# Optimization experiments

Hardware: AMD Instinct MI355X
Metric: run time of the kernel (lower is better)

Reference implementation:

```python
import jax, jax.numpy as jnp
import numpy as np

N_POWER_SERIES = 8  # 'fixed' estimator, n_power_series=8, n_samples=4 (leading axis of v)


def _g_fn(x, W1, b1, W2, b2):
    # residual branch g(x): Linear -> ELU -> Linear (canonical i-ResNet block)
    return jax.nn.elu(x @ W1 + b1) @ W2 + b2


def setup_inputs() -> dict:
    key = jax.random.key(0)
    ks = jax.random.split(key, 4)
    B, D, H, S = 8192, 1024, 4096, 4
    x = jax.random.normal(ks[0], (B, D), jnp.float32)
    # scale weights so g is roughly contractive (Lipschitz < 1), as spectral norm enforces
    W1 = jax.random.normal(ks[1], (D, H), jnp.float32) * (0.5 / np.sqrt(D))
    b1 = jnp.zeros((H,), jnp.float32)
    W2 = jax.random.normal(ks[2], (H, D), jnp.float32) * (0.5 / np.sqrt(H))
    b2 = jnp.zeros((D,), jnp.float32)
    v = jax.random.normal(ks[3], (S, B, D), jnp.float32)  # Hutchinson probes
    log_df_dz = jnp.zeros((B,), jnp.float32)
    return {"x": x, "log_df_dz": log_df_dz, "W1": W1, "b1": b1, "W2": W2, "b2": b2, "v": v}


def reference(x, log_df_dz, W1, b1, W2, b2, v):
    g, vjp_fn = jax.vjp(lambda xx: _g_fn(xx, W1, b1, W2, b2), x)
    vjp = lambda w: vjp_fn(w)[0]  # w^T J, w: [B, D]

    w = v                      # [S, B, D]
    sum_diag = jnp.zeros(v.shape[:2], v.dtype)  # [S, B]
    for k in range(1, N_POWER_SERIES + 1):
        w = jax.vmap(vjp)(w)                        # v^T J^k
        inner = jnp.einsum('sbd,sbd->sb', w, v)     # Hutchinson tr(J^k) estimate
        sign = 1.0 if (k % 2 == 1) else -1.0
        sum_diag = sum_diag + sign * (inner / k)
    logdet = jnp.mean(sum_diag, axis=0)             # mean over samples -> [B]

    z = x + g
    return z, log_df_dz + logdet
```

## Files before the change

### kernel.cpp

```cpp
#include <hip/hip_runtime.h>
#include <hip/hip_bf16.h>

using bf16 = __hip_bfloat16;
typedef __attribute__((ext_vector_type(8))) short bf16x8;
typedef __attribute__((ext_vector_type(4))) float f32x4;

__device__ __forceinline__ float b2f(unsigned short u) {
  union { unsigned int i; float f; } x; x.i = ((unsigned int)u) << 16; return x.f;
}
__device__ __forceinline__ unsigned short f2b(float f) {
  __hip_bfloat16 h = __float2bfloat16(f);
  return *reinterpret_cast<unsigned short*>(&h);
}

__device__ __forceinline__ void load16_to_lds(const bf16* g, void* lds) {
  __builtin_amdgcn_global_load_lds((const __attribute__((address_space(1))) void*)g,
                                   (__attribute__((address_space(3))) void*)lds, 16, 0, 0);
}

#define FENCE() asm volatile("" ::: "memory")
#define BAR() do { FENCE(); __builtin_amdgcn_s_barrier(); FENCE(); } while (0)

__global__ void cast_f32_bf16(const float* __restrict__ in, bf16* __restrict__ out, size_t n) {
  size_t i0 = ((size_t)blockIdx.x * 256 + threadIdx.x) * 4;
  size_t stride = (size_t)gridDim.x * 256 * 4;
  for (size_t i = i0; i < n; i += stride) {
    float4 f = *(const float4*)(in + i);
    ushort4 o;
    o.x = f2b(f.x); o.y = f2b(f.y); o.z = f2b(f.z); o.w = f2b(f.w);
    *(ushort4*)(out + i) = o;
  }
}

__global__ void transpose_cast(const float* __restrict__ in, bf16* __restrict__ out, int R, int C) {
  __shared__ float tile[32][33];
  int tx = threadIdx.x & 31, ty = threadIdx.x >> 5;
  int r0 = blockIdx.y * 32, c0 = blockIdx.x * 32;
  #pragma unroll
  for (int i = 0; i < 32; i += 8)
    tile[ty + i][tx] = in[(size_t)(r0 + ty + i) * C + (c0 + tx)];
  __syncthreads();
  #pragma unroll
  for (int i = 0; i < 32; i += 8)
    out[(size_t)(c0 + ty + i) * R + (r0 + tx)] = __float2bfloat16(tile[tx][ty + i]);
}

template<int EPI>
__global__ __launch_bounds__(512, 2)
void gemm256(const bf16* __restrict__ A, const bf16* __restrict__ Bm,
             int M, int N, int K,
             bf16* __restrict__ OutB,
             const float* __restrict__ bias,
             const bf16* __restrict__ Ea) {
  __shared__ __align__(16) char pool[131072];
  char* Albs = pool;
  char* Blbs = pool + 65536;
  const int tid = threadIdx.x;
  const int l = tid & 63, w = tid >> 6;
  const int lane16 = l & 15, lh = l >> 4;
  const int wr = w >> 2, wc = w & 3;
  const int bm0 = blockIdx.y * 256, bn0 = blockIdx.x * 256;
  const int nkt = K >> 6, NT2 = nkt >> 1;

  auto stage = [&](const bf16* G, int grow0, int kbase, char* ldsbase) {
    #pragma unroll
    for (int r = 0; r < 2; ++r) {
      int p = (r * 512 + tid) * 16;
      int row = p >> 7, colb = p & 127;
      int cs = colb ^ ((row & 7) << 4);
      const bf16* g = G + (size_t)(grow0 + row) * K + kbase + (cs >> 1);
      load16_to_lds(g, ldsbase + (size_t)(r * 512 + w * 64) * 16);
    }
  };
  auto rd = [&](const char* base, int row, int colb) -> bf16x8 {
    return *(const bf16x8*)(base + row * 128 + (colb ^ ((row & 7) << 4)));
  };

  f32x4 acc[8][4] = {};
  bf16x8 a_r[4][2], b_r[4][2];

  #define RD_A(mq, buf) { _Pragma("unroll") for (int i = 0; i < 4; ++i) \
      _Pragma("unroll") for (int kk = 0; kk < 2; ++kk) \
      a_r[i][kk] = rd(Albs + (buf) * 32768, wr * 128 + (mq) * 64 + i * 16 + lane16, kk * 64 + lh * 16); }
  #define RD_B(buf) { _Pragma("unroll") for (int nf = 0; nf < 4; ++nf) \
      _Pragma("unroll") for (int kk = 0; kk < 2; ++kk) \
      b_r[nf][kk] = rd(Blbs + (buf) * 32768, wc * 64 + nf * 16 + lane16, kk * 64 + lh * 16); }
  #define MFMA_H(mq, n0) { __builtin_amdgcn_s_setprio(1); \
      _Pragma("unroll") for (int i = 0; i < 4; ++i) \
      _Pragma("unroll") for (int nn = 0; nn < 2; ++nn) \
      _Pragma("unroll") for (int kk = 0; kk < 2; ++kk) \
        acc[(mq)*4+i][(n0)+nn] = __builtin_amdgcn_mfma_f32_16x16x32_bf16( \
            a_r[i][kk], b_r[(n0)+nn][kk], acc[(mq)*4+i][(n0)+nn], 0, 0, 0); \
      __builtin_amdgcn_s_setprio(0); }

  stage(Bm, bn0 + 0,   0,  Blbs + 0);
  stage(Bm, bn0 + 128, 0,  Blbs + 16384);
  stage(A,  bm0 + 0,   0,  Albs + 0);
  stage(A,  bm0 + 128, 0,  Albs + 16384);
  stage(Bm, bn0 + 0,   64, Blbs + 32768);
  stage(Bm, bn0 + 128, 64, Blbs + 32768 + 16384);
  stage(A,  bm0 + 0,   64, Albs + 32768);
  asm volatile("s_waitcnt vmcnt(6)" ::: "memory");
  BAR();

  for (int t = 0; t < NT2; ++t) {
    const int k2 = (2 * t + 2) * 64, k3 = (2 * t + 3) * 64;
    const bool nl = (t < NT2 - 1);
    RD_B(0); RD_A(0, 0);
    stage(A, bm0 + 128, (2 * t + 1) * 64, Albs + 32768 + 16384);
    BAR();
    MFMA_H(0, 0);
    BAR();
    if (nl) stage(Bm, bn0 + 0, k2, Blbs + 0);
    BAR();
    MFMA_H(0, 2);
    BAR();
    RD_A(1, 0);
    if (nl) stage(Bm, bn0 + 128, k2, Blbs + 16384);
    BAR();
    MFMA_H(1, 0);
    BAR();
    if (nl) stage(A, bm0 + 0, k2, Albs + 0);
    BAR();
    MFMA_H(1, 2);
    if (nl) { asm volatile("s_waitcnt vmcnt(6)" ::: "memory"); }
    else    { asm volatile("s_waitcnt vmcnt(0)" ::: "memory"); }
    BAR();
    RD_B(1); RD_A(0, 1);
    if (nl) stage(A, bm0 + 128, k2, Albs + 16384);
    BAR();
    MFMA_H(0, 0);
    BAR();
    if (nl) stage(Bm, bn0 + 0, k3, Blbs + 32768);
    BAR();
    MFMA_H(0, 2);
    BAR();
    RD_A(1, 1);
    if (nl) stage(Bm, bn0 + 128, k3, Blbs + 32768 + 16384);
    BAR();
    MFMA_H(1, 0);
    BAR();
    if (nl) stage(A, bm0 + 0, k3, Albs + 32768);
    BAR();
    MFMA_H(1, 2);
    if (nl) { asm volatile("s_waitcnt vmcnt(6)" ::: "memory"); }
    BAR();
  }

  float* scr = (float*)(pool + w * 4352);
  const int row0 = bm0 + wr * 128, col0 = bn0 + wc * 64;
  #pragma unroll
  for (int mf = 0; mf < 8; ++mf) {
    #pragma unroll
    for (int nf = 0; nf < 4; ++nf)
      #pragma unroll
      for (int q = 0; q < 4; ++q)
        scr[(lh * 4 + q) * 68 + nf * 16 + lane16] = acc[mf][nf][q];
    #pragma unroll
    for (int p = 0; p < 2; ++p) {
      int row = p * 8 + (l >> 3);
      int c0 = (l & 7) * 8;
      const float* sp = &scr[row * 68 + c0];
      f32x4 lo = *(const f32x4*)sp;
      f32x4 hi = *(const f32x4*)(sp + 4);
      int gm = row0 + mf * 16 + row;
      int gn = col0 + c0;
      size_t idx = (size_t)gm * N + gn;
      bf16x8 ov;
      if (EPI == 0) {
        f32x4 b0 = *(const f32x4*)&bias[gn];
        f32x4 b1 = *(const f32x4*)&bias[gn + 4];
        #pragma unroll
        for (int j = 0; j < 8; ++j) {
          float fj = (j < 4) ? lo[j] : hi[j - 4];
          float bj = (j < 4) ? b0[j] : b1[j - 4];
          float hv = fj + bj;
          float a = hv > 0.f ? hv : expm1f(hv);
          ov[j] = (short)f2b(a);
        }
      } else {
        bf16x8 ea = *(const bf16x8*)&Ea[idx];
        #pragma unroll
        for (int j = 0; j < 8; ++j) {
          float fj = (j < 4) ? lo[j] : hi[j - 4];
          float a = b2f((unsigned short)ea[j]);
          float e = a > 0.f ? 1.f : a + 1.f;
          ov[j] = (short)f2b(fj * e);
        }
      }
      *(bf16x8*)(&OutB[idx]) = ov;
    }
    FENCE();
  }
  #undef RD_A
  #undef RD_B
  #undef MFMA_H
}

template<int EPI>
__global__ __launch_bounds__(256)
void gemm_bt(const bf16* __restrict__ A, const bf16* __restrict__ Bm,
             int M, int N, int K,
             bf16* __restrict__ OutB, float* __restrict__ OutF,
             const float* __restrict__ bias, const float* __restrict__ Xadd) {
  __shared__ __align__(16) char pool[4 * 4352];
  bf16* As = (bf16*)pool;
  bf16* Bs = (bf16*)(pool + 8192);
  const int tid = threadIdx.x;
  const int l = tid & 63, w = tid >> 6;
  const int wr = w >> 1, wc = w & 1;
  const int lane16 = l & 15, lh = l >> 4;
  const int bm0 = blockIdx.y * 128, bn0 = blockIdx.x * 128;

  f32x4 acc[4][4] = {};
  const int nk = K >> 5;
  for (int kt = 0; kt < nk; ++kt) {
    const size_t kbase = (size_t)kt * 32;
    #pragma unroll
    for (int i = 0; i < 2; ++i) {
      int c = i * 256 + w * 64 + l;
      int row = c >> 2, cb = (c & 3) << 3;
      const bf16* ga = A  + (size_t)(bm0 + row) * K + kbase + cb;
      const bf16* gb = Bm + (size_t)(bn0 + row) * K + kbase + cb;
      char* la = (char*)As + (size_t)(i * 256 + w * 64) * 16;
      char* lb = (char*)Bs + (size_t)(i * 256 + w * 64) * 16;
      load16_to_lds(ga, la);
      load16_to_lds(gb, lb);
    }
    __syncthreads();
    bf16x8 af[4], bfv[4];
    #pragma unroll
    for (int r = 0; r < 4; ++r)
      af[r] = *(const bf16x8*)&As[(wr * 64 + r * 16 + lane16) * 32 + lh * 8];
    #pragma unroll
    for (int c = 0; c < 4; ++c)
      bfv[c] = *(const bf16x8*)&Bs[(wc * 64 + c * 16 + lane16) * 32 + lh * 8];
    #pragma unroll
    for (int r = 0; r < 4; ++r)
      #pragma unroll
      for (int c = 0; c < 4; ++c)
        acc[r][c] = __builtin_amdgcn_mfma_f32_16x16x32_bf16(af[r], bfv[c], acc[r][c], 0, 0, 0);
    __syncthreads();
  }

  if (EPI == 1) {
    #pragma unroll
    for (int r = 0; r < 4; ++r) {
      int gm_base = bm0 + wr * 64 + r * 16 + lh * 4;
      #pragma unroll
      for (int c = 0; c < 4; ++c) {
        int gn = bn0 + wc * 64 + c * 16 + lane16;
        #pragma unroll
        for (int q = 0; q < 4; ++q) {
          size_t idx = (size_t)(gm_base + q) * N + gn;
          OutF[idx] = acc[r][c][q] + bias[gn] + Xadd[idx];
        }
      }
    }
  } else {
    float* scr = (float*)(pool + w * 4352);
    #pragma unroll
    for (int r = 0; r < 4; ++r) {
      #pragma unroll
      for (int c = 0; c < 4; ++c)
        #pragma unroll
        for (int q = 0; q < 4; ++q)
          scr[(lh * 4 + q) * 68 + c * 16 + lane16] = acc[r][c][q];
      #pragma unroll
      for (int p = 0; p < 2; ++p) {
        int row = p * 8 + (l >> 3);
        int c0 = (l & 7) * 8;
        const float* sp = &scr[row * 68 + c0];
        f32x4 lo = *(const f32x4*)sp;
        f32x4 hi = *(const f32x4*)(sp + 4);
        int gm = bm0 + wr * 64 + r * 16 + row;
        int gn = bn0 + wc * 64 + c0;
        size_t idx = (size_t)gm * N + gn;
        bf16x8 ov;
        #pragma unroll
        for (int j = 0; j < 8; ++j) {
          float fj = (j < 4) ? lo[j] : hi[j - 4];
          ov[j] = (short)f2b(fj);
        }
        *(bf16x8*)(&OutB[idx]) = ov;
      }
      __syncthreads();
    }
  }
}

__global__ void rowdot(const bf16* __restrict__ W, const float* __restrict__ V,
                       float* __restrict__ sumdiag, float coef, int D) {
  size_t row = blockIdx.x;
  const unsigned short* wr = (const unsigned short*)W + row * D;
  const float* vr = V + row * D;
  int t = threadIdx.x;
  float s = 0.f;
  for (int i = t * 4; i < D; i += 256 * 4) {
    ushort4 a = *(const ushort4*)(wr + i);
    float4  b = *(const float4*)(vr + i);
    s += b2f(a.x) * b.x + b2f(a.y) * b.y + b2f(a.z) * b.z + b2f(a.w) * b.w;
  }
  #pragma unroll
  for (int o = 32; o > 0; o >>= 1) s += __shfl_down(s, o);
  __shared__ float red[4];
  if ((t & 63) == 0) red[t >> 6] = s;
  __syncthreads();
  if (t == 0) sumdiag[row] += coef * (red[0] + red[1] + red[2] + red[3]);
}

__global__ void finalize(const float* __restrict__ ldz, const float* __restrict__ sd,
                         float* __restrict__ out, int B, int S) {
  int b = blockIdx.x * 256 + threadIdx.x;
  if (b >= B) return;
  float acc = 0.f;
  for (int s = 0; s < S; ++s) acc += sd[(size_t)s * B + b];
  out[b] = ldz[b] + acc / (float)S;
}

extern "C" void kernel_launch(void* const* d_in, const int* in_sizes, int n_in,
                              void* d_out, int out_size, void* d_ws, size_t ws_size,
                              hipStream_t stream) {
  const int B = 8192, D = 1024, H = 4096, S = 4, NPS = 8;
  const float* x   = (const float*)d_in[0];
  const float* ldz = (const float*)d_in[1];
  const float* W1  = (const float*)d_in[2];
  const float* b1  = (const float*)d_in[3];
  const float* W2  = (const float*)d_in[4];
  const float* b2  = (const float*)d_in[5];
  const float* v   = (const float*)d_in[6];
  float* z_out  = (float*)d_out;
  float* ld_out = z_out + (size_t)B * D;

  char* ws = (char*)d_ws;
  size_t off = 0;
  auto alloc = [&](size_t bytes) {
    char* p = ws + off; off = (off + bytes + 255) & ~(size_t)255; return p;
  };
  float* sumdiag = (float*)alloc((size_t)S * B * 4);
  bf16* W1b  = (bf16*)alloc((size_t)D * H * 2);
  bf16* W2b  = (bf16*)alloc((size_t)D * H * 2);
  bf16* W1T  = (bf16*)alloc((size_t)D * H * 2);
  bf16* W2T  = (bf16*)alloc((size_t)D * H * 2);
  bf16* xb   = (bf16*)alloc((size_t)B * D * 2);
  bf16* abuf = (bf16*)alloc((size_t)B * H * 2);
  bf16* tbuf = (bf16*)alloc((size_t)B * H * 2);
  (void)ws_size; (void)in_sizes; (void)n_in; (void)out_size;

  hipMemsetAsync(sumdiag, 0, (size_t)S * B * 4, stream);

  cast_f32_bf16<<<1024, 256, 0, stream>>>(x,  xb,  (size_t)B * D);
  cast_f32_bf16<<<1024, 256, 0, stream>>>(W1, W1b, (size_t)D * H);
  cast_f32_bf16<<<1024, 256, 0, stream>>>(W2, W2b, (size_t)D * H);
  transpose_cast<<<dim3(H / 32, D / 32), 256, 0, stream>>>(W1, W1T, D, H);
  transpose_cast<<<dim3(D / 32, H / 32), 256, 0, stream>>>(W2, W2T, H, D);

  gemm256<0><<<dim3(H / 256, B / 256), 512, 0, stream>>>(xb, W1T, B, H, D,
      abuf, b1, nullptr);
  gemm_bt<1><<<dim3(D / 128, B / 128), 256, 0, stream>>>(abuf, W2T, B, D, H,
      nullptr, z_out, b2, x);

  bf16* wcur = xb;
  for (int s = 0; s < S; ++s) {
    const float* vs = v + (size_t)s * B * D;
    cast_f32_bf16<<<1024, 256, 0, stream>>>(vs, wcur, (size_t)B * D);
    for (int k = 1; k <= NPS; ++k) {
      gemm256<2><<<dim3(H / 256, B / 256), 512, 0, stream>>>(wcur, W2b, B, H, D,
          tbuf, nullptr, abuf);
      gemm_bt<3><<<dim3(D / 128, B / 128), 256, 0, stream>>>(tbuf, W1b, B, D, H,
          wcur, nullptr, nullptr, nullptr);
      float coef = ((k & 1) ? 1.f : -1.f) / (float)k;
      rowdot<<<B, 256, 0, stream>>>(wcur, vs, sumdiag + (size_t)s * B, coef, D);
    }
  }
  finalize<<<B / 256, 256, 0, stream>>>(ldz, sumdiag, ld_out, B, S);
}
```

Before: 6.425 ms.

## Move ELU-derivative multiply into second GEMM prologue and pin MFMA scheduling

The ELU-derivative gating (t * elu'(a)) moves out of the epilogue of the first backward GEMM and into the A-tile load of the second GEMM. There the tile is read through registers, multiplied by the derivative and written to LDS, instead of using the direct global-to-LDS load. The main-loop phases of gemm256 are also wrapped in sched_barrier pins so the compiler cannot interleave MFMAs with the LDS reads or staging. This removes the extra Ea read from gemm256's epilogue, but gemm_bt's A path becomes synchronous register loads, and Ea is now read once per output-column block instead of once.

```diff
diff --git a/kernel.cpp b/kernel.cpp
--- a/kernel.cpp
+++ b/kernel.cpp
@@ -20,6 +20,7 @@
 
 #define FENCE() asm volatile("" ::: "memory")
 #define BAR() do { FENCE(); __builtin_amdgcn_s_barrier(); FENCE(); } while (0)
+#define SCHED_PIN() __builtin_amdgcn_sched_barrier(0)
 
 __global__ void cast_f32_bf16(const float* __restrict__ in, bf16* __restrict__ out, size_t n) {
   size_t i0 = ((size_t)blockIdx.x * 256 + threadIdx.x) * 4;
@@ -50,8 +51,7 @@
 void gemm256(const bf16* __restrict__ A, const bf16* __restrict__ Bm,
              int M, int N, int K,
              bf16* __restrict__ OutB,
-             const float* __restrict__ bias,
-             const bf16* __restrict__ Ea) {
+             const float* __restrict__ bias) {
   __shared__ __align__(16) char pool[131072];
   char* Albs = pool;
   char* Blbs = pool + 65536;
@@ -60,7 +60,7 @@
   const int lane16 = l & 15, lh = l >> 4;
   const int wr = w >> 2, wc = w & 3;
   const int bm0 = blockIdx.y * 256, bn0 = blockIdx.x * 256;
-  const int nkt = K >> 6, NT2 = nkt >> 1;
+  const int NT2 = K >> 7;
 
   auto stage = [&](const bf16* G, int grow0, int kbase, char* ldsbase) {
     #pragma unroll
@@ -92,6 +92,7 @@
         acc[(mq)*4+i][(n0)+nn] = __builtin_amdgcn_mfma_f32_16x16x32_bf16( \
             a_r[i][kk], b_r[(n0)+nn][kk], acc[(mq)*4+i][(n0)+nn], 0, 0, 0); \
       __builtin_amdgcn_s_setprio(0); }
+  #define PHASE(BODY_PRE, MFMA_CALL) { BODY_PRE; BAR(); SCHED_PIN(); MFMA_CALL; SCHED_PIN(); BAR(); }
 
   stage(Bm, bn0 + 0,   0,  Blbs + 0);
   stage(Bm, bn0 + 128, 0,  Blbs + 16384);
@@ -101,50 +102,29 @@
   stage(Bm, bn0 + 128, 64, Blbs + 32768 + 16384);
   stage(A,  bm0 + 0,   64, Albs + 32768);
   asm volatile("s_waitcnt vmcnt(6)" ::: "memory");
+  SCHED_PIN();
   BAR();
 
   for (int t = 0; t < NT2; ++t) {
     const int k2 = (2 * t + 2) * 64, k3 = (2 * t + 3) * 64;
     const bool nl = (t < NT2 - 1);
-    RD_B(0); RD_A(0, 0);
-    stage(A, bm0 + 128, (2 * t + 1) * 64, Albs + 32768 + 16384);
-    BAR();
-    MFMA_H(0, 0);
-    BAR();
-    if (nl) stage(Bm, bn0 + 0, k2, Blbs + 0);
-    BAR();
-    MFMA_H(0, 2);
-    BAR();
-    RD_A(1, 0);
-    if (nl) stage(Bm, bn0 + 128, k2, Blbs + 16384);
-    BAR();
-    MFMA_H(1, 0);
-    BAR();
-    if (nl) stage(A, bm0 + 0, k2, Albs + 0);
-    BAR();
-    MFMA_H(1, 2);
-    if (nl) { asm volatile("s_waitcnt vmcnt(6)" ::: "memory"); }
-    else    { asm volatile("s_waitcnt vmcnt(0)" ::: "memory"); }
-    BAR();
-    RD_B(1); RD_A(0, 1);
-    if (nl) stage(A, bm0 + 128, k2, Albs + 16384);
-    BAR();
-    MFMA_H(0, 0);
-    BAR();
-    if (nl) stage(Bm, bn0 + 0, k3, Blbs + 32768);
-    BAR();
-    MFMA_H(0, 2);
-    BAR();
-    RD_A(1, 1);
-    if (nl) stage(Bm, bn0 + 128, k3, Blbs + 32768 + 16384);
-    BAR();
-    MFMA_H(1, 0);
-    BAR();
-    if (nl) stage(A, bm0 + 0, k3, Albs + 32768);
-    BAR();
-    MFMA_H(1, 2);
-    if (nl) { asm volatile("s_waitcnt vmcnt(6)" ::: "memory"); }
-    BAR();
+    PHASE({ RD_B(0); RD_A(0, 0); stage(A, bm0 + 128, (2 * t + 1) * 64, Albs + 32768 + 16384); },
+          MFMA_H(0, 0));
+    PHASE({ if (nl) stage(Bm, bn0 + 0, k2, Blbs + 0); }, MFMA_H(0, 2));
+    PHASE({ RD_A(1, 0); if (nl) stage(Bm, bn0 + 128, k2, Blbs + 16384); }, MFMA_H(1, 0));
+    { if (nl) stage(A, bm0 + 0, k2, Albs + 0);
+      BAR(); SCHED_PIN(); MFMA_H(1, 2); SCHED_PIN();
+      if (nl) { asm volatile("s_waitcnt vmcnt(6)" ::: "memory"); }
+      else    { asm volatile("s_waitcnt vmcnt(0)" ::: "memory"); }
+      SCHED_PIN(); BAR(); }
+    PHASE({ RD_B(1); RD_A(0, 1); if (nl) stage(A, bm0 + 128, k2, Albs + 16384); },
+          MFMA_H(0, 0));
+    PHASE({ if (nl) stage(Bm, bn0 + 0, k3, Blbs + 32768); }, MFMA_H(0, 2));
+    PHASE({ RD_A(1, 1); if (nl) stage(Bm, bn0 + 128, k3, Blbs + 32768 + 16384); }, MFMA_H(1, 0));
+    { if (nl) stage(A, bm0 + 0, k3, Albs + 32768);
+      BAR(); SCHED_PIN(); MFMA_H(1, 2); SCHED_PIN();
+      if (nl) { asm volatile("s_waitcnt vmcnt(6)" ::: "memory"); }
+      SCHED_PIN(); BAR(); }
   }
 
   float* scr = (float*)(pool + w * 4352);
@@ -179,13 +159,10 @@
           ov[j] = (short)f2b(a);
         }
       } else {
-        bf16x8 ea = *(const bf16x8*)&Ea[idx];
         #pragma unroll
         for (int j = 0; j < 8; ++j) {
           float fj = (j < 4) ? lo[j] : hi[j - 4];
-          float a = b2f((unsigned short)ea[j]);
-          float e = a > 0.f ? 1.f : a + 1.f;
-          ov[j] = (short)f2b(fj * e);
+          ov[j] = (short)f2b(fj);
         }
       }
       *(bf16x8*)(&OutB[idx]) = ov;
@@ -195,6 +172,7 @@
   #undef RD_A
   #undef RD_B
   #undef MFMA_H
+  #undef PHASE
 }
 
 template<int EPI>
@@ -202,7 +180,8 @@
 void gemm_bt(const bf16* __restrict__ A, const bf16* __restrict__ Bm,
              int M, int N, int K,
              bf16* __restrict__ OutB, float* __restrict__ OutF,
-             const float* __restrict__ bias, const float* __restrict__ Xadd) {
+             const float* __restrict__ bias, const float* __restrict__ Xadd,
+             const bf16* __restrict__ Ea) {
   __shared__ __align__(16) char pool[4 * 4352];
   bf16* As = (bf16*)pool;
   bf16* Bs = (bf16*)(pool + 8192);
@@ -220,12 +199,28 @@
     for (int i = 0; i < 2; ++i) {
       int c = i * 256 + w * 64 + l;
       int row = c >> 2, cb = (c & 3) << 3;
-      const bf16* ga = A  + (size_t)(bm0 + row) * K + kbase + cb;
       const bf16* gb = Bm + (size_t)(bn0 + row) * K + kbase + cb;
-      char* la = (char*)As + (size_t)(i * 256 + w * 64) * 16;
       char* lb = (char*)Bs + (size_t)(i * 256 + w * 64) * 16;
-      load16_to_lds(ga, la);
       load16_to_lds(gb, lb);
+      if (EPI == 3) {
+        const bf16* ga = A  + (size_t)(bm0 + row) * K + kbase + cb;
+        const bf16* ge = Ea + (size_t)(bm0 + row) * K + kbase + cb;
+        bf16x8 tv = *(const bf16x8*)ga;
+        bf16x8 av = *(const bf16x8*)ge;
+        bf16x8 o;
+        #pragma unroll
+        for (int j = 0; j < 8; ++j) {
+          float tj = b2f((unsigned short)tv[j]);
+          float aj = b2f((unsigned short)av[j]);
+          float e = aj > 0.f ? 1.f : aj + 1.f;
+          o[j] = (short)f2b(tj * e);
+        }
+        *(bf16x8*)&As[(size_t)c * 8] = o;
+      } else {
+        const bf16* ga = A + (size_t)(bm0 + row) * K + kbase + cb;
+        char* la = (char*)As + (size_t)(i * 256 + w * 64) * 16;
+        load16_to_lds(ga, la);
+      }
     }
     __syncthreads();
     bf16x8 af[4], bfv[4];
@@ -355,20 +350,19 @@
   transpose_cast<<<dim3(H / 32, D / 32), 256, 0, stream>>>(W1, W1T, D, H);
   transpose_cast<<<dim3(D / 32, H / 32), 256, 0, stream>>>(W2, W2T, H, D);
 
-  gemm256<0><<<dim3(H / 256, B / 256), 512, 0, stream>>>(xb, W1T, B, H, D,
-      abuf, b1, nullptr);
+  gemm256<0><<<dim3(H / 256, B / 256), 512, 0, stream>>>(xb, W1T, B, H, D, abuf, b1);
   gemm_bt<1><<<dim3(D / 128, B / 128), 256, 0, stream>>>(abuf, W2T, B, D, H,
-      nullptr, z_out, b2, x);
+      nullptr, z_out, b2, x, nullptr);
 
   bf16* wcur = xb;
   for (int s = 0; s < S; ++s) {
     const float* vs = v + (size_t)s * B * D;
     cast_f32_bf16<<<1024, 256, 0, stream>>>(vs, wcur, (size_t)B * D);
     for (int k = 1; k <= NPS; ++k) {
-      gemm256<2><<<dim3(H / 256, B / 256), 512, 0, stream>>>(wcur, W2b, B, H, D,
-          tbuf, nullptr, abuf);
+      gemm256<3><<<dim3(H / 256, B / 256), 512, 0, stream>>>(wcur, W2b, B, H, D,
+          tbuf, nullptr);
       gemm_bt<3><<<dim3(D / 128, B / 128), 256, 0, stream>>>(tbuf, W1b, B, D, H,
-          wcur, nullptr, nullptr, nullptr);
+          wcur, nullptr, nullptr, nullptr, abuf);
       float coef = ((k & 1) ? 1.f : -1.f) / (float)k;
       rowdot<<<B, 256, 0, stream>>>(wcur, vs, sumdiag + (size_t)s * B, coef, D);
     }
```

Result: slower. 12.85 ms (+99.9%).
